# Kernel tuning notes

Hardware: AMD Instinct MI355X
Metric: run time of the kernel (lower is better)

The kernel has to match this reference:

```python
import jax, jax.numpy as jnp
import numpy as np

N_COMPONENTS = 8
N_DIMENSIONS = 16
N_POINTS = 500000


def setup_inputs() -> dict:
    key = jax.random.key(0)
    k1, k2, k3 = jax.random.split(key, 3)
    data = jax.random.normal(k1, (N_POINTS, N_DIMENSIONS), dtype=jnp.float32)
    logits = jnp.ones((N_COMPONENTS,), dtype=jnp.float32)
    means = jax.random.normal(k2, (N_COMPONENTS, N_DIMENSIONS), dtype=jnp.float32)
    scales = jax.random.normal(k3, (N_COMPONENTS, N_DIMENSIONS, N_DIMENSIONS), dtype=jnp.float32)
    return {"data": data, "logits": logits, "means": means, "scales": scales}


def _gmm_log_prob(data, logits, means, scales):
    # covariances = scales @ scales^T  -> [K, D, D]
    covs = jnp.einsum('kij,klj->kil', scales, scales)
    L = jnp.linalg.cholesky(covs)  # [K, D, D]
    # diff: [K, N, D]
    diff = data[None, :, :] - means[:, None, :]
    # solve L y = diff^T  -> y: [K, D, N]
    y = jax.scipy.linalg.solve_triangular(L, jnp.swapaxes(diff, 1, 2), lower=True)
    maha = jnp.sum(y * y, axis=1)  # [K, N]
    half_logdet = jnp.sum(jnp.log(jnp.diagonal(L, axis1=1, axis2=2)), axis=-1)  # [K]
    D = data.shape[-1]
    log2pi = jnp.float32(np.log(2.0 * np.pi))
    comp_lp = -0.5 * (maha + D * log2pi) - half_logdet[:, None]  # [K, N]
    mix_lp = jax.nn.log_softmax(logits)  # [K]
    return jax.scipy.special.logsumexp(mix_lp[:, None] + comp_lp, axis=0)  # [N]


def reference(data, logits, means, scales):
    return _gmm_log_prob(data, logits, means, scales)
```

## Files before the change

### kernel.cpp

```cpp
#include <hip/hip_runtime.h>
#include <math.h>

#define KC 8
#define DD 16
#define BLK 256

typedef short short8 __attribute__((ext_vector_type(8)));
typedef float floatx16 __attribute__((ext_vector_type(16)));

__device__ __forceinline__ unsigned asu(float x) { return __float_as_uint(x); }

__global__ __launch_bounds__(128) void gmm_prep(
    const float* __restrict__ logits,
    const float* __restrict__ means,
    const float* __restrict__ scales,
    uint4* __restrict__ AH2,
    uint4* __restrict__ AL2,
    float* __restrict__ BF,
    float* __restrict__ Cout)
{
    const int tid  = threadIdx.x;
    const int k    = tid >> 4;
    const int i    = tid & 15;
    const int lane = tid & 63;
    const int base = lane & 48;

    float srow[DD];
    {
        const float4* sp = (const float4*)(scales + (size_t)(k * DD + i) * DD);
#pragma unroll
        for (int q = 0; q < 4; ++q) {
            float4 v = sp[q];
            srow[4 * q + 0] = v.x; srow[4 * q + 1] = v.y;
            srow[4 * q + 2] = v.z; srow[4 * q + 3] = v.w;
        }
    }

    float a[DD];
#pragma unroll
    for (int j = 0; j < DD; ++j) a[j] = 0.f;
#pragma unroll
    for (int d = 0; d < DD; ++d) {
        float sid = srow[d];
#pragma unroll
        for (int j = 0; j < DD; ++j) {
            float sjd = __shfl(srow[d], base + j, 64);
            a[j] = fmaf(sid, sjd, a[j]);
        }
    }

    float l[DD];
    float hld = 0.f;
#pragma unroll
    for (int j = 0; j < DD; ++j) {
        float ajj = __shfl(a[j], base + j, 64);
        float ljj = sqrtf(ajj);
        hld += logf(ljj);
        float lij = (i < j) ? 0.f : (a[j] / ljj);
        l[j] = lij;
#pragma unroll
        for (int c = j + 1; c < DD; ++c) {
            float lcj = __shfl(l[j], base + c, 64);
            a[c] = fmaf(-lij, lcj, a[c]);
        }
    }

    float xc[DD];
#pragma unroll
    for (int r = 0; r < DD; ++r) {
        float s = (r == i) ? 1.f : 0.f;
#pragma unroll
        for (int t = 0; t < DD; ++t) {
            if (t < r) {
                float lrt = __shfl(l[t], base + r, 64);
                s = fmaf(-lrt, xc[t], s);
            }
        }
        float lrr = __shfl(l[r], base + r, 64);
        xc[r] = (r < i) ? 0.f : (s / lrr);
    }

    __shared__ float Ash[KC][DD][DD + 1];
#pragma unroll
    for (int r = 0; r < DD; ++r) Ash[k][r][i] = xc[r];
    __syncthreads();

    float rowA[DD];
    float bb = 0.f;
#pragma unroll
    for (int j = 0; j < DD; ++j) {
        float aij = Ash[k][i][j];
        rowA[j] = aij;
        bb = fmaf(aij, means[k * DD + j], bb);
    }

    const int P = k >> 1;
    const int m = (k & 1) * 16 + i;
#pragma unroll
    for (int h = 0; h < 2; ++h) {
        unsigned dh[4], dl[4];
#pragma unroll
        for (int jj = 0; jj < 4; ++jj) {
            float e = rowA[h * 8 + 2 * jj];
            float o = rowA[h * 8 + 2 * jj + 1];
            unsigned he = asu(e) & 0xFFFF0000u, ho = asu(o) & 0xFFFF0000u;
            float re = e - __uint_as_float(he);
            float ro = o - __uint_as_float(ho);
            dh[jj] = (he >> 16) | ho;
            dl[jj] = ((asu(re) & 0xFFFF0000u) >> 16) | (asu(ro) & 0xFFFF0000u);
        }
        AH2[P * 64 + h * 32 + m] = make_uint4(dh[0], dh[1], dh[2], dh[3]);
        AL2[P * 64 + h * 32 + m] = make_uint4(dl[0], dl[1], dl[2], dl[3]);
    }

    {
        const int h = (m >> 2) & 1;
        const int t = (m & 3) | ((m >> 3) << 2);
        BF[P * 32 + h * 16 + t] = -bb;
    }

    if (i == 0) {
        float mx = logits[0];
        for (int t = 1; t < KC; ++t) mx = fmaxf(mx, logits[t]);
        float se = 0.f;
        for (int t = 0; t < KC; ++t) se += expf(logits[t] - mx);
        float lse = mx + logf(se);
        const float log2pi = 1.8378770664093453f;
        Cout[k] = (logits[k] - lse) - hld - 0.5f * DD * log2pi;
    }
}

__global__ __launch_bounds__(BLK, 4) void gmm_lp(
    const float* __restrict__ data,
    const uint4* __restrict__ AH2,
    const uint4* __restrict__ AL2,
    const float* __restrict__ BF,
    const float* __restrict__ Cg,
    float* __restrict__ out, int N)
{
    const int tid  = threadIdx.x;
    const int lane = tid & 63;
    const int half = lane >> 5;
    const int wbase = blockIdx.x * BLK + (tid & ~63);

    short8 bh[2], bl[2];
#pragma unroll
    for (int s = 0; s < 2; ++s) {
        int p = wbase + s * 32 + (lane & 31);
        p = p < N ? p : N - 1;
        const float4* xp = (const float4*)(data + (size_t)p * DD + half * 8);
        float4 v0 = xp[0], v1 = xp[1];
        float xs[8] = {v0.x, v0.y, v0.z, v0.w, v1.x, v1.y, v1.z, v1.w};
        unsigned dh[4], dl[4];
#pragma unroll
        for (int jj = 0; jj < 4; ++jj) {
            float e = xs[2 * jj], o = xs[2 * jj + 1];
            unsigned he = asu(e) & 0xFFFF0000u, ho = asu(o) & 0xFFFF0000u;
            float re = e - __uint_as_float(he);
            float ro = o - __uint_as_float(ho);
            dh[jj] = __builtin_amdgcn_perm(ho, he, 0x07060302u);
            dl[jj] = __builtin_amdgcn_perm(asu(ro), asu(re), 0x07060302u);
        }
        bh[s] = __builtin_bit_cast(short8, make_uint4(dh[0], dh[1], dh[2], dh[3]));
        bl[s] = __builtin_bit_cast(short8, make_uint4(dl[0], dl[1], dl[2], dl[3]));
    }

    float mx = -1e30f, sum = 0.f;

#pragma unroll 1
    for (int P = 0; P < 4; ++P) {
        short8 ah = __builtin_bit_cast(short8, AH2[P * 64 + lane]);
        short8 al = __builtin_bit_cast(short8, AL2[P * 64 + lane]);
        const float4* bfp = (const float4*)(BF + P * 32 + half * 16);
        float4 b0 = bfp[0], b1 = bfp[1], b2 = bfp[2], b3 = bfp[3];
        float ck0 = Cg[2 * P], ck1 = Cg[2 * P + 1];

        float me[2], mo[2];
#pragma unroll
        for (int s = 0; s < 2; ++s) {
            floatx16 acc = {b0.x, b0.y, b0.z, b0.w, b1.x, b1.y, b1.z, b1.w,
                            b2.x, b2.y, b2.z, b2.w, b3.x, b3.y, b3.z, b3.w};
            acc = __builtin_amdgcn_mfma_f32_32x32x16_bf16(ah, bh[s], acc, 0, 0, 0);
            acc = __builtin_amdgcn_mfma_f32_32x32x16_bf16(ah, bl[s], acc, 0, 0, 0);
            acc = __builtin_amdgcn_mfma_f32_32x32x16_bf16(al, bh[s], acc, 0, 0, 0);
            float se = acc[0] * acc[0], so = acc[8] * acc[8];
#pragma unroll
            for (int t = 1; t < 8; ++t) {
                se = fmaf(acc[t], acc[t], se);
                so = fmaf(acc[t + 8], acc[t + 8], so);
            }
            me[s] = se + __shfl_xor(se, 32, 64);
            mo[s] = so + __shfl_xor(so, 32, 64);
        }

        float mE = half ? me[1] : me[0];
        float mO = half ? mo[1] : mo[0];

        float lpk = fmaf(-0.5f, mE, ck0);
        float nm = fmaxf(mx, lpk);
        sum = sum * __expf(mx - nm) + __expf(lpk - nm);
        mx = nm;

        lpk = fmaf(-0.5f, mO, ck1);
        nm = fmaxf(mx, lpk);
        sum = sum * __expf(mx - nm) + __expf(lpk - nm);
        mx = nm;
    }

    const int id = wbase + lane;
    if (id < N) out[id] = mx + __logf(sum);
}

extern "C" void kernel_launch(void* const* d_in, const int* in_sizes, int n_in,
                              void* d_out, int out_size, void* d_ws, size_t ws_size,
                              hipStream_t stream) {
    const float* data   = (const float*)d_in[0];
    const float* logits = (const float*)d_in[1];
    const float* means  = (const float*)d_in[2];
    const float* scales = (const float*)d_in[3];
    float* out = (float*)d_out;
    const int N = in_sizes[0] / DD;

    uint4* AH2 = (uint4*)d_ws;
    uint4* AL2 = AH2 + 4 * 64;
    float* BF  = (float*)(AL2 + 4 * 64);
    float* C   = BF + 128;

    gmm_prep<<<1, 128, 0, stream>>>(logits, means, scales, AH2, AL2, BF, C);
    const int nblk = (N + BLK - 1) / BLK;
    gmm_lp<<<nblk, BLK, 0, stream>>>(data, AH2, AL2, BF, C, out, N);
}
```

Before: 92.33 us.

## Fuse Cholesky prep into main kernel, recompute per block into shared memory

Removes the separate single-block prep kernel and instead has every block redundantly compute the covariance Cholesky factors, inverse, bias and constants, then stage them in shared memory for the MFMA loop. This eliminates one kernel launch and the serialized dependency on a tiny prep kernel. In exchange each of roughly 2000 blocks repeats the shuffle-heavy 16x16 Cholesky and triangular inverse, and shared memory use grows, which may hurt occupancy.

```diff
diff --git a/kernel.cpp b/kernel.cpp
--- a/kernel.cpp
+++ b/kernel.cpp
@@ -10,138 +10,135 @@
 
 __device__ __forceinline__ unsigned asu(float x) { return __float_as_uint(x); }
 
-__global__ __launch_bounds__(128) void gmm_prep(
+__global__ __launch_bounds__(BLK, 4) void gmm_fused(
+    const float* __restrict__ data,
     const float* __restrict__ logits,
     const float* __restrict__ means,
     const float* __restrict__ scales,
-    uint4* __restrict__ AH2,
-    uint4* __restrict__ AL2,
-    float* __restrict__ BF,
-    float* __restrict__ Cout)
-{
-    const int tid  = threadIdx.x;
-    const int k    = tid >> 4;
-    const int i    = tid & 15;
-    const int lane = tid & 63;
-    const int base = lane & 48;
-
-    float srow[DD];
-    {
-        const float4* sp = (const float4*)(scales + (size_t)(k * DD + i) * DD);
-#pragma unroll
-        for (int q = 0; q < 4; ++q) {
-            float4 v = sp[q];
-            srow[4 * q + 0] = v.x; srow[4 * q + 1] = v.y;
-            srow[4 * q + 2] = v.z; srow[4 * q + 3] = v.w;
-        }
-    }
-
-    float a[DD];
-#pragma unroll
-    for (int j = 0; j < DD; ++j) a[j] = 0.f;
-#pragma unroll
-    for (int d = 0; d < DD; ++d) {
-        float sid = srow[d];
-#pragma unroll
-        for (int j = 0; j < DD; ++j) {
-            float sjd = __shfl(srow[d], base + j, 64);
-            a[j] = fmaf(sid, sjd, a[j]);
-        }
-    }
-
-    float l[DD];
-    float hld = 0.f;
-#pragma unroll
-    for (int j = 0; j < DD; ++j) {
-        float ajj = __shfl(a[j], base + j, 64);
-        float ljj = sqrtf(ajj);
-        hld += logf(ljj);
-        float lij = (i < j) ? 0.f : (a[j] / ljj);
-        l[j] = lij;
-#pragma unroll
-        for (int c = j + 1; c < DD; ++c) {
-            float lcj = __shfl(l[j], base + c, 64);
-            a[c] = fmaf(-lij, lcj, a[c]);
-        }
-    }
-
-    float xc[DD];
-#pragma unroll
-    for (int r = 0; r < DD; ++r) {
-        float s = (r == i) ? 1.f : 0.f;
-#pragma unroll
-        for (int t = 0; t < DD; ++t) {
-            if (t < r) {
-                float lrt = __shfl(l[t], base + r, 64);
-                s = fmaf(-lrt, xc[t], s);
-            }
-        }
-        float lrr = __shfl(l[r], base + r, 64);
-        xc[r] = (r < i) ? 0.f : (s / lrr);
-    }
-
-    __shared__ float Ash[KC][DD][DD + 1];
-#pragma unroll
-    for (int r = 0; r < DD; ++r) Ash[k][r][i] = xc[r];
-    __syncthreads();
-
-    float rowA[DD];
-    float bb = 0.f;
-#pragma unroll
-    for (int j = 0; j < DD; ++j) {
-        float aij = Ash[k][i][j];
-        rowA[j] = aij;
-        bb = fmaf(aij, means[k * DD + j], bb);
-    }
-
-    const int P = k >> 1;
-    const int m = (k & 1) * 16 + i;
-#pragma unroll
-    for (int h = 0; h < 2; ++h) {
-        unsigned dh[4], dl[4];
-#pragma unroll
-        for (int jj = 0; jj < 4; ++jj) {
-            float e = rowA[h * 8 + 2 * jj];
-            float o = rowA[h * 8 + 2 * jj + 1];
-            unsigned he = asu(e) & 0xFFFF0000u, ho = asu(o) & 0xFFFF0000u;
-            float re = e - __uint_as_float(he);
-            float ro = o - __uint_as_float(ho);
-            dh[jj] = (he >> 16) | ho;
-            dl[jj] = ((asu(re) & 0xFFFF0000u) >> 16) | (asu(ro) & 0xFFFF0000u);
-        }
-        AH2[P * 64 + h * 32 + m] = make_uint4(dh[0], dh[1], dh[2], dh[3]);
-        AL2[P * 64 + h * 32 + m] = make_uint4(dl[0], dl[1], dl[2], dl[3]);
-    }
-
-    {
-        const int h = (m >> 2) & 1;
-        const int t = (m & 3) | ((m >> 3) << 2);
-        BF[P * 32 + h * 16 + t] = -bb;
-    }
-
-    if (i == 0) {
-        float mx = logits[0];
-        for (int t = 1; t < KC; ++t) mx = fmaxf(mx, logits[t]);
-        float se = 0.f;
-        for (int t = 0; t < KC; ++t) se += expf(logits[t] - mx);
-        float lse = mx + logf(se);
-        const float log2pi = 1.8378770664093453f;
-        Cout[k] = (logits[k] - lse) - hld - 0.5f * DD * log2pi;
-    }
-}
-
-__global__ __launch_bounds__(BLK, 4) void gmm_lp(
-    const float* __restrict__ data,
-    const uint4* __restrict__ AH2,
-    const uint4* __restrict__ AL2,
-    const float* __restrict__ BF,
-    const float* __restrict__ Cg,
     float* __restrict__ out, int N)
 {
+    __shared__ float Ash[KC][DD][DD + 1];
+    __shared__ uint4 sAH[4 * 64];
+    __shared__ uint4 sAL[4 * 64];
+    __shared__ __align__(16) float sBF[128];
+    __shared__ float sC[KC];
+
     const int tid  = threadIdx.x;
     const int lane = tid & 63;
     const int half = lane >> 5;
     const int wbase = blockIdx.x * BLK + (tid & ~63);
+
+    const int k    = (tid >> 4) & 7;
+    const int i    = tid & 15;
+    const int base = lane & 48;
+
+    float xc[DD];
+    float hld = 0.f;
+    {
+        float srow[DD];
+        {
+            const float4* sp = (const float4*)(scales + (size_t)(k * DD + i) * DD);
+#pragma unroll
+            for (int q = 0; q < 4; ++q) {
+                float4 v = sp[q];
+                srow[4 * q + 0] = v.x; srow[4 * q + 1] = v.y;
+                srow[4 * q + 2] = v.z; srow[4 * q + 3] = v.w;
+            }
+        }
+
+        float a[DD];
+#pragma unroll
+        for (int j = 0; j < DD; ++j) a[j] = 0.f;
+#pragma unroll
+        for (int d = 0; d < DD; ++d) {
+            float sid = srow[d];
+#pragma unroll
+            for (int j = 0; j < DD; ++j) {
+                float sjd = __shfl(srow[d], base + j, 64);
+                a[j] = fmaf(sid, sjd, a[j]);
+            }
+        }
+
+        float l[DD];
+#pragma unroll
+        for (int j = 0; j < DD; ++j) {
+            float ajj = __shfl(a[j], base + j, 64);
+            float ljj = sqrtf(ajj);
+            hld += logf(ljj);
+            float lij = (i < j) ? 0.f : (a[j] / ljj);
+            l[j] = lij;
+#pragma unroll
+            for (int c = j + 1; c < DD; ++c) {
+                float lcj = __shfl(l[j], base + c, 64);
+                a[c] = fmaf(-lij, lcj, a[c]);
+            }
+        }
+
+#pragma unroll
+        for (int r = 0; r < DD; ++r) {
+            float s = (r == i) ? 1.f : 0.f;
+#pragma unroll
+            for (int t = 0; t < DD; ++t) {
+                if (t < r) {
+                    float lrt = __shfl(l[t], base + r, 64);
+                    s = fmaf(-lrt, xc[t], s);
+                }
+            }
+            float lrr = __shfl(l[r], base + r, 64);
+            xc[r] = (r < i) ? 0.f : (s / lrr);
+        }
+    }
+
+#pragma unroll
+    for (int r = 0; r < DD; ++r) Ash[k][r][i] = xc[r];
+    __syncthreads();
+
+    {
+        float rowA[DD];
+        float bb = 0.f;
+#pragma unroll
+        for (int j = 0; j < DD; ++j) {
+            float aij = Ash[k][i][j];
+            rowA[j] = aij;
+            bb = fmaf(aij, means[k * DD + j], bb);
+        }
+
+        const int P = k >> 1;
+        const int m = (k & 1) * 16 + i;
+#pragma unroll
+        for (int h = 0; h < 2; ++h) {
+            unsigned dh[4], dl[4];
+#pragma unroll
+            for (int jj = 0; jj < 4; ++jj) {
+                float e = rowA[h * 8 + 2 * jj];
+                float o = rowA[h * 8 + 2 * jj + 1];
+                unsigned he = asu(e) & 0xFFFF0000u, ho = asu(o) & 0xFFFF0000u;
+                float re = e - __uint_as_float(he);
+                float ro = o - __uint_as_float(ho);
+                dh[jj] = (he >> 16) | ho;
+                dl[jj] = ((asu(re) & 0xFFFF0000u) >> 16) | (asu(ro) & 0xFFFF0000u);
+            }
+            sAH[P * 64 + h * 32 + m] = make_uint4(dh[0], dh[1], dh[2], dh[3]);
+            sAL[P * 64 + h * 32 + m] = make_uint4(dl[0], dl[1], dl[2], dl[3]);
+        }
+
+        {
+            const int h = (m >> 2) & 1;
+            const int t = (m & 3) | ((m >> 3) << 2);
+            sBF[P * 32 + h * 16 + t] = -bb;
+        }
+
+        if (i == 0) {
+            float mxl = logits[0];
+            for (int t = 1; t < KC; ++t) mxl = fmaxf(mxl, logits[t]);
+            float se = 0.f;
+            for (int t = 0; t < KC; ++t) se += expf(logits[t] - mxl);
+            float lse = mxl + logf(se);
+            const float log2pi = 1.8378770664093453f;
+            sC[k] = (logits[k] - lse) - hld - 0.5f * DD * log2pi;
+        }
+    }
+    __syncthreads();
 
     short8 bh[2], bl[2];
 #pragma unroll
@@ -169,11 +166,11 @@
 
 #pragma unroll 1
     for (int P = 0; P < 4; ++P) {
-        short8 ah = __builtin_bit_cast(short8, AH2[P * 64 + lane]);
-        short8 al = __builtin_bit_cast(short8, AL2[P * 64 + lane]);
-        const float4* bfp = (const float4*)(BF + P * 32 + half * 16);
+        short8 ah = __builtin_bit_cast(short8, sAH[P * 64 + lane]);
+        short8 al = __builtin_bit_cast(short8, sAL[P * 64 + lane]);
+        const float4* bfp = (const float4*)(sBF + P * 32 + half * 16);
         float4 b0 = bfp[0], b1 = bfp[1], b2 = bfp[2], b3 = bfp[3];
-        float ck0 = Cg[2 * P], ck1 = Cg[2 * P + 1];
+        float ck0 = sC[2 * P], ck1 = sC[2 * P + 1];
 
         float me[2], mo[2];
 #pragma unroll
@@ -221,12 +218,6 @@
     float* out = (float*)d_out;
     const int N = in_sizes[0] / DD;
 
-    uint4* AH2 = (uint4*)d_ws;
-    uint4* AL2 = AH2 + 4 * 64;
-    float* BF  = (float*)(AL2 + 4 * 64);
-    float* C   = BF + 128;
-
-    gmm_prep<<<1, 128, 0, stream>>>(logits, means, scales, AH2, AL2, BF, C);
     const int nblk = (N + BLK - 1) / BLK;
-    gmm_lp<<<nblk, BLK, 0, stream>>>(data, AH2, AL2, BF, C, out, N);
+    gmm_fused<<<nblk, BLK, 0, stream>>>(data, logits, means, scales, out, N);
 }
```

New measurement: 134.3 us. 45.4% more time.
